# Optimization experiments

Measured on AMD Instinct MI355X. Metric: run time of the kernel, lower is better.

The kernel has to match this reference:

```python
import jax, jax.numpy as jnp
import numpy as np

IMAGE_SIZE = (128, 128)
NUM_SLICES = 4
SLICE_SPACING = 0.1
BACKGROUND = 0.0
CHUNK = 1024
N_GAUSS = 4096
EPS = 1e-6


def setup_inputs() -> dict:
    key = jax.random.key(0)
    k1, k2, k3, k4, k5 = jax.random.split(key, 5)
    return {
        "means": jax.random.uniform(k1, (N_GAUSS, 3), dtype=jnp.float32),
        "scales": jax.random.uniform(k2, (N_GAUSS, 3), dtype=jnp.float32),
        "rotations": jax.random.normal(k3, (N_GAUSS, 4), dtype=jnp.float32),
        "opacities": jax.random.uniform(k4, (N_GAUSS, 1), dtype=jnp.float32),
        "features": jax.random.uniform(k5, (N_GAUSS, 1), dtype=jnp.float32),
    }


def _quat_to_rot(q):
    # q: [N,4] (w,x,y,z) -> [N,3,3]
    q = q / jnp.linalg.norm(q, axis=1, keepdims=True)
    w, x, y, z = q[:, 0], q[:, 1], q[:, 2], q[:, 3]
    r0 = jnp.stack([1 - 2 * (y * y + z * z), 2 * (x * y - w * z), 2 * (x * z + w * y)], axis=-1)
    r1 = jnp.stack([2 * (x * y + w * z), 1 - 2 * (x * x + z * z), 2 * (y * z - w * x)], axis=-1)
    r2 = jnp.stack([2 * (x * z - w * y), 2 * (y * z + w * x), 1 - 2 * (x * x + y * y)], axis=-1)
    return jnp.stack([r0, r1, r2], axis=-2)


def _forward(means, scales, rotations, opacities, features):
    H, W = IMAGE_SIZE
    dtype = means.dtype
    P = H * W

    # 3D covariance: Sigma = (R S)(R S)^T
    R = _quat_to_rot(rotations)
    RS = R * scales[:, None, :]
    cov = RS @ jnp.swapaxes(RS, 1, 2)  # [N,3,3]

    # slice z positions and shared pixel grid
    total_depth = (NUM_SLICES - 1) * SLICE_SPACING
    zs = jnp.linspace(-total_depth / 2, total_depth / 2, NUM_SLICES)
    yy, xx = jnp.meshgrid(jnp.linspace(-1, 1, H), jnp.linspace(-1, 1, W), indexing="ij")
    grid = jnp.stack([xx, yy], axis=-1).reshape(P, 2).astype(dtype)

    # conditional (marginal-at-z) 2D covariance, slice independent
    sxy = cov[:, :2, :2]                     # [N,2,2]
    sxz = cov[:, :2, 2]                      # [N,2]
    szz = cov[:, 2, 2]                       # [N]
    sigma2d = sxy - (sxz[:, :, None] * sxz[:, None, :]) / (szz + EPS)[:, None, None]
    sigma2d = sigma2d + EPS * jnp.eye(2, dtype=dtype)
    a, b = sigma2d[:, 0, 0], sigma2d[:, 0, 1]
    c, d = sigma2d[:, 1, 0], sigma2d[:, 1, 1]
    det = a * d - b * c
    inv2d = jnp.stack([jnp.stack([d, -b], -1), jnp.stack([-c, a], -1)], -2) / det[:, None, None]

    max_dist = 3.0 * scales[:, 2].max()

    nch = N_GAUSS // CHUNK
    rs = lambda t: t.reshape((nch, CHUNK) + t.shape[1:])
    chunks = (rs(means), rs(inv2d), rs(sxz), rs(szz), rs(opacities[:, 0]), rs(features[:, 0]))

    def render_slice(slice_z):
        def body(carry, ch):
            img, acc = carry
            mu, invk, sxzk, szzk, op, ft = ch
            mask = (jnp.abs(mu[:, 2] - slice_z) < max_dist).astype(dtype)  # all-pass by construction
            zoff = slice_z - mu[:, 2]
            mu2d = mu[:, :2] + sxzk / (szzk + EPS)[:, None] * zoff[:, None]  # [K,2]
            off = grid[:, None, :] - mu2d[None, :, :]                        # [P,K,2]
            maha = jnp.einsum("pki,kij,pkj->pk", off, invk, off)
            g = jnp.exp(-0.5 * maha) * mask[None, :]                         # [P,K]
            weight = (1 - acc)[:, None] * (g * op[None, :])
            img = img + (weight * (g * ft[None, :])).sum(-1)
            acc = acc + weight.sum(-1)
            return (img, acc), None

        init = (jnp.zeros(P, dtype), jnp.zeros(P, dtype))
        (img, acc), _ = jax.lax.scan(body, init, chunks)
        img = img + (1 - acc) * BACKGROUND
        return img.reshape(H, W)

    return jnp.stack([render_slice(zs[s]) for s in range(NUM_SLICES)], axis=0)


def reference(means, scales, rotations, opacities, features):
    return _forward(means, scales, rotations, opacities, features)
```

## Files before the change

### kernel.cpp

```cpp
#include <hip/hip_runtime.h>


#define EPSV 1e-6f
#define NG   4096
#define PP   16384
#define NSL  4
#define GSEG 128
#define SUBB 16

__global__ void prep_kernel(const float* __restrict__ means,
                            const float* __restrict__ scales,
                            const float* __restrict__ rots,
                            const float* __restrict__ ops,
                            const float* __restrict__ fts,
                            float4* __restrict__ gdata) {
    __shared__ float red[256];
    int tid = threadIdx.x;

    float m = -1e30f;
    for (int i = tid; i < NG; i += 256) m = fmaxf(m, scales[i*3+2]);
    red[tid] = m;
    __syncthreads();
    for (int s = 128; s > 0; s >>= 1) {
        if (tid < s) red[tid] = fmaxf(red[tid], red[tid+s]);
        __syncthreads();
    }
    float maxd = 3.0f * red[0];

    int g = blockIdx.x * 256 + tid;
    if (g >= NG) return;

    float qw = rots[g*4+0], qx = rots[g*4+1], qy = rots[g*4+2], qz = rots[g*4+3];
    float inorm = rsqrtf(qw*qw + qx*qx + qy*qy + qz*qz);
    qw *= inorm; qx *= inorm; qy *= inorm; qz *= inorm;

    float s0 = scales[g*3+0], s1 = scales[g*3+1], s2 = scales[g*3+2];

    float r00 = 1.f - 2.f*(qy*qy + qz*qz), r01 = 2.f*(qx*qy - qw*qz), r02 = 2.f*(qx*qz + qw*qy);
    float r10 = 2.f*(qx*qy + qw*qz), r11 = 1.f - 2.f*(qx*qx + qz*qz), r12 = 2.f*(qy*qz - qw*qx);
    float r20 = 2.f*(qx*qz - qw*qy), r21 = 2.f*(qy*qz + qw*qx), r22 = 1.f - 2.f*(qx*qx + qy*qy);

    float a00 = r00*s0, a01 = r01*s1, a02 = r02*s2;
    float a10 = r10*s0, a11 = r11*s1, a12 = r12*s2;
    float a20 = r20*s0, a21 = r21*s1, a22 = r22*s2;

    float c00 = a00*a00 + a01*a01 + a02*a02;
    float c01 = a00*a10 + a01*a11 + a02*a12;
    float c02 = a00*a20 + a01*a21 + a02*a22;
    float c11 = a10*a10 + a11*a11 + a12*a12;
    float c12 = a10*a20 + a11*a21 + a12*a22;
    float c22 = a20*a20 + a21*a21 + a22*a22;

    float izz = 1.0f / (c22 + EPSV);
    float kx = c02 * izz, ky = c12 * izz;
    float sa = c00 - c02*c02*izz + EPSV;
    float sb = c01 - c02*c12*izz;
    float sd = c11 - c12*c12*izz + EPSV;
    float det = sa*sd - sb*sb;
    float idet = 1.0f / det;

    const float C0 = -0.72134752044448170f;
    float qa = C0 * sd * idet;
    float qb = C0 * (-2.0f * sb * idet);
    float qd = C0 * sa * idet;

    float mx = means[g*3+0], my = means[g*3+1], mz = means[g*3+2];
    float op = ops[g], ft = fts[g];

    #pragma unroll
    for (int s = 0; s < NSL; ++s) {
        float z = -0.15f + 0.1f * (float)s;
        float zoff = z - mz;
        float m2x = mx + kx * zoff;
        float m2y = my + ky * zoff;
        bool live = (fabsf(mz - z) < maxd) && (op > 1e-12f);
        float lop  = live ? __log2f(op) : -__builtin_inff();
        float ftop = live ? ft / op     : 0.f;
        float c3 = -(2.0f*qa*m2x + qb*m2y);
        float c4 = -(2.0f*qd*m2y + qb*m2x);
        float c5 = qa*m2x*m2x + qb*m2x*m2y + qd*m2y*m2y + lop;
        float4* o = gdata + ((size_t)(s*NG + g)) * 2;
        o[0] = make_float4(qa, qb, qd, c3);
        o[1] = make_float4(c4, c5, ftop, 0.f);
    }
}

__global__ __launch_bounds__(512, 8)
void render_kernel(const float4* __restrict__ gdata, float2* __restrict__ part) {
    int tid   = threadIdx.x;
    int lane  = tid & 63;
    int w     = __builtin_amdgcn_readfirstlane(tid >> 6);
    int b     = blockIdx.x;
    int cs    = b & 31;
    int band  = b >> 5;
    int slice = band >> 3;
    int r0    = (band & 7) * 16 + w * 2;

    const float DL = 2.0f / 127.0f;
    float x0 = -1.0f + (float)lane * DL;
    float x1 = x0 + 64.0f * DL;
    float y0 = -1.0f + (float)r0 * DL;
    float y1 = y0 + DL;

    const float4* base = gdata + ((size_t)slice * NG + cs * GSEG) * 2;

    float a100 = 0.f, a101 = 0.f, a110 = 0.f, a111 = 0.f;
    float a200 = 0.f, a201 = 0.f, a210 = 0.f, a211 = 0.f;

    for (int kk = 0; kk < 8; ++kk) {
        int sb = (w + kk) & 7;
        const float4* q = base + sb * SUBB * 2;
        #pragma unroll 8
        for (int j = 0; j < SUBB; ++j) {
            float4 A = q[2*j+0];
            float4 B = q[2*j+1];
            float T0 = fmaf(A.y, y0, A.w);
            float T1 = fmaf(A.y, y1, A.w);
            float R0 = fmaf(fmaf(A.z, y0, B.x), y0, B.y);
            float R1 = fmaf(fmaf(A.z, y1, B.x), y1, B.y);
            float m00 = fmaf(fmaf(A.x, x0, T0), x0, R0);
            float m01 = fmaf(fmaf(A.x, x1, T0), x1, R0);
            float m10 = fmaf(fmaf(A.x, x0, T1), x0, R1);
            float m11 = fmaf(fmaf(A.x, x1, T1), x1, R1);
            float g00 = __builtin_amdgcn_exp2f(m00);
            float g01 = __builtin_amdgcn_exp2f(m01);
            float g10 = __builtin_amdgcn_exp2f(m10);
            float g11 = __builtin_amdgcn_exp2f(m11);
            a100 += g00;  a101 += g01;  a110 += g10;  a111 += g11;
            a200 = fmaf(g00*g00, B.z, a200);
            a201 = fmaf(g01*g01, B.z, a201);
            a210 = fmaf(g10*g10, B.z, a210);
            a211 = fmaf(g11*g11, B.z, a211);
        }
    }

    size_t o = (size_t)cs * (NSL * PP) + slice * PP + r0 * 128 + lane;
    part[o      ] = make_float2(a100, a200);
    part[o +  64] = make_float2(a101, a201);
    part[o + 128] = make_float2(a110, a210);
    part[o + 192] = make_float2(a111, a211);
}

__global__ __launch_bounds__(256)
void combine_kernel(const float2* __restrict__ part, float* __restrict__ out) {
    int px = blockIdx.x * 256 + threadIdx.x;
    float img = 0.f, acc = 0.f;
    #pragma unroll
    for (int c = 0; c < 4; ++c) {
        float S1 = 0.f, S2 = 0.f;
        #pragma unroll
        for (int s = 0; s < 8; ++s) {
            float2 v = part[(size_t)(c*8 + s) * (NSL*PP) + px];
            S1 += v.x;  S2 += v.y;
        }
        float om = 1.0f - acc;
        img = fmaf(om, S2, img);
        acc = fmaf(om, S1, acc);
    }
    out[px] = img;
}

extern "C" void kernel_launch(void* const* d_in, const int* in_sizes, int n_in,
                              void* d_out, int out_size, void* d_ws, size_t ws_size,
                              hipStream_t stream) {
    const float* means  = (const float*)d_in[0];
    const float* scales = (const float*)d_in[1];
    const float* rots   = (const float*)d_in[2];
    const float* ops    = (const float*)d_in[3];
    const float* fts    = (const float*)d_in[4];
    float* out = (float*)d_out;

    float4* gdata = (float4*)d_ws;
    float2* part  = (float2*)((char*)d_ws + (size_t)NSL*NG*32);

    prep_kernel<<<NG/256, 256, 0, stream>>>(means, scales, rots, ops, fts, gdata);
    render_kernel<<<1024, 512, 0, stream>>>(gdata, part);
    combine_kernel<<<NSL*PP/256, 256, 0, stream>>>(part, out);
}
```

Baseline: 128.9 us.

## Render 8 rows per thread with per-column factored quadratic, halve grid

Each thread now covers one x column and eight rows instead of a 2x2 pixel tile. The x-dependent part of the quadratic form is computed once per gaussian and reused across all eight rows. This lowers the FMA count per pixel and amortizes each gaussian load over more pixels. The grid is halved and the launch bound relaxed to 4 waves, trading occupancy for more registers and more work per thread.

```diff
diff --git a/kernel.cpp b/kernel.cpp
--- a/kernel.cpp
+++ b/kernel.cpp
@@ -85,7 +85,7 @@
     }
 }
 
-__global__ __launch_bounds__(512, 8)
+__global__ __launch_bounds__(512, 4)
 void render_kernel(const float4* __restrict__ gdata, float2* __restrict__ part) {
     int tid   = threadIdx.x;
     int lane  = tid & 63;
@@ -93,52 +93,49 @@
     int b     = blockIdx.x;
     int cs    = b & 31;
     int band  = b >> 5;
-    int slice = band >> 3;
-    int r0    = (band & 7) * 16 + w * 2;
+    int slice = band >> 2;
+    int ch    = w & 1;
+    int rbase = (band & 3) * 32 + (w >> 1) * 8;
 
     const float DL = 2.0f / 127.0f;
-    float x0 = -1.0f + (float)lane * DL;
-    float x1 = x0 + 64.0f * DL;
-    float y0 = -1.0f + (float)r0 * DL;
-    float y1 = y0 + DL;
+    float x = -1.0f + (float)(ch * 64 + lane) * DL;
+
+    float yv[8];
+    #pragma unroll
+    for (int j = 0; j < 8; ++j) yv[j] = -1.0f + (float)(rbase + j) * DL;
 
     const float4* base = gdata + ((size_t)slice * NG + cs * GSEG) * 2;
 
-    float a100 = 0.f, a101 = 0.f, a110 = 0.f, a111 = 0.f;
-    float a200 = 0.f, a201 = 0.f, a210 = 0.f, a211 = 0.f;
+    float s1[8], s2[8];
+    #pragma unroll
+    for (int j = 0; j < 8; ++j) { s1[j] = 0.f; s2[j] = 0.f; }
 
     for (int kk = 0; kk < 8; ++kk) {
         int sb = (w + kk) & 7;
         const float4* q = base + sb * SUBB * 2;
         #pragma unroll 8
-        for (int j = 0; j < SUBB; ++j) {
-            float4 A = q[2*j+0];
-            float4 B = q[2*j+1];
-            float T0 = fmaf(A.y, y0, A.w);
-            float T1 = fmaf(A.y, y1, A.w);
-            float R0 = fmaf(fmaf(A.z, y0, B.x), y0, B.y);
-            float R1 = fmaf(fmaf(A.z, y1, B.x), y1, B.y);
-            float m00 = fmaf(fmaf(A.x, x0, T0), x0, R0);
-            float m01 = fmaf(fmaf(A.x, x1, T0), x1, R0);
-            float m10 = fmaf(fmaf(A.x, x0, T1), x0, R1);
-            float m11 = fmaf(fmaf(A.x, x1, T1), x1, R1);
-            float g00 = __builtin_amdgcn_exp2f(m00);
-            float g01 = __builtin_amdgcn_exp2f(m01);
-            float g10 = __builtin_amdgcn_exp2f(m10);
-            float g11 = __builtin_amdgcn_exp2f(m11);
-            a100 += g00;  a101 += g01;  a110 += g10;  a111 += g11;
-            a200 = fmaf(g00*g00, B.z, a200);
-            a201 = fmaf(g01*g01, B.z, a201);
-            a210 = fmaf(g10*g10, B.z, a210);
-            a211 = fmaf(g11*g11, B.z, a211);
+        for (int t = 0; t < SUBB; ++t) {
+            float4 A = q[2*t+0];
+            float4 B = q[2*t+1];
+            float A1 = fmaf(A.x, x, A.w);
+            float A2 = fmaf(A.y, x, B.x);
+            float A3 = fmaf(A1,  x, B.y);
+            #pragma unroll
+            for (int j = 0; j < 8; ++j) {
+                float wj = fmaf(A.z, yv[j], A2);
+                float mj = fmaf(wj, yv[j], A3);
+                float gj = __builtin_amdgcn_exp2f(mj);
+                s1[j] += gj;
+                s2[j] = fmaf(gj * gj, B.z, s2[j]);
+            }
         }
     }
 
-    size_t o = (size_t)cs * (NSL * PP) + slice * PP + r0 * 128 + lane;
-    part[o      ] = make_float2(a100, a200);
-    part[o +  64] = make_float2(a101, a201);
-    part[o + 128] = make_float2(a110, a210);
-    part[o + 192] = make_float2(a111, a211);
+    size_t ob = (size_t)cs * (NSL * PP) + (size_t)slice * PP
+              + (size_t)rbase * 128 + ch * 64 + lane;
+    #pragma unroll
+    for (int j = 0; j < 8; ++j)
+        part[ob + (size_t)j * 128] = make_float2(s1[j], s2[j]);
 }
 
 __global__ __launch_bounds__(256)
@@ -174,6 +171,6 @@
     float2* part  = (float2*)((char*)d_ws + (size_t)NSL*NG*32);
 
     prep_kernel<<<NG/256, 256, 0, stream>>>(means, scales, rots, ops, fts, gdata);
-    render_kernel<<<1024, 512, 0, stream>>>(gdata, part);
+    render_kernel<<<512, 512, 0, stream>>>(gdata, part);
     combine_kernel<<<NSL*PP/256, 256, 0, stream>>>(part, out);
 }
```

Measured after the change: 121.0 us. 1.07x faster.
